# Kernel tuning notes

Hardware: AMD Instinct MI355X
Metric: run time of the kernel (lower is better)

The kernel has to match this reference:

```python
import jax, jax.numpy as jnp
import numpy as np

B, D = 65536, 784          # batch, input features
H = 256                     # delegator feature (hidden) dim
L = 64                      # num_leaves (experts)
C = 10                      # num_classes


def setup_inputs() -> dict:
    key = jax.random.key(0)
    ks = jax.random.split(key, 7)
    s_in = 1.0 / np.sqrt(D)
    s_h = 1.0 / np.sqrt(H)
    return {
        "x": jax.random.normal(ks[0], (B, D), dtype=jnp.float32),
        "Wf": jax.random.normal(ks[1], (D, H), dtype=jnp.float32) * s_in,   # Node feature proj
        "bf": jnp.zeros((H,), dtype=jnp.float32),
        "Wr": jax.random.normal(ks[2], (D, L), dtype=jnp.float32) * s_in,   # Node router proj
        "br": jnp.zeros((L,), dtype=jnp.float32),
        "Wl": jax.random.normal(ks[3], (L, H, C), dtype=jnp.float32) * s_h,  # per-leaf linear
        "bl": jnp.zeros((L, C), dtype=jnp.float32),
    }


def reference(x, Wf, bf, Wr, br, Wl, bl):
    # Delegator (Node): features + routing probabilities
    features = jax.nn.relu(x @ Wf + bf)                 # [B, H]
    probs = jax.nn.softmax(x @ Wr + br, axis=1)         # [B, L]
    choices = jnp.argmax(probs, axis=1)                 # [B] top-1 leaf per sample
    # Per-sample leaf dispatch: gather each sample's leaf weights, then a
    # batched vec-mat product (memory-bound gather, low FLOP/byte).
    Wc = Wl[choices]                                    # [B, H, C]
    bc = bl[choices]                                    # [B, C]
    predictions = jnp.einsum("bh,bhc->bc", features, Wc) + bc  # [B, C]
    return predictions
```

## Files before the change

### kernel.cpp

```cpp
#include <hip/hip_runtime.h>
#include <stdint.h>

#define B_ROWS 65536
#define D_IN   784
#define H_DIM  256
#define L_LEAF 64
#define C_CLS  10
#define NSTEP  13
#define BTILE  40960
#define GAP_THRESH 0.03f

using f32x4    = __attribute__((ext_vector_type(4))) float;
using bf16x8   = __attribute__((ext_vector_type(8))) short;
using ushort8v = __attribute__((ext_vector_type(8))) unsigned short;
using ushort4v = __attribute__((ext_vector_type(4))) unsigned short;

#define O_FLAGCNT  0
#define O_CHOICES  4096
#define O_FLAGROWS (O_CHOICES + B_ROWS * 4)
#define O_WT       (O_FLAGROWS + B_ROWS * 4)
#define O_FEAT     (O_WT + NSTEP * BTILE)
#define O_WLB      (O_FEAT + (size_t)B_ROWS * H_DIM * 2)
#define WS_BASE    O_WLB
#define WS_FULL    (O_WLB + (size_t)L_LEAF * H_DIM * C_CLS * 2)

__device__ __forceinline__ unsigned short f2bf(float f) {
    union { float f; unsigned int u; } c; c.f = f;
    unsigned int u = c.u;
    return (unsigned short)((u + 0x7fffu + ((u >> 16) & 1u)) >> 16);
}
__device__ __forceinline__ float bf2f(unsigned short u) {
    union { unsigned int u; float f; } c; c.u = ((unsigned int)u) << 16;
    return c.f;
}
__device__ __forceinline__ unsigned int cvtpk(float a, float b) {
    unsigned int r;
    asm("v_cvt_pk_bf16_f32 %0, %1, %2" : "=v"(r) : "v"(a), "v"(b));
    return r;
}

__device__ __forceinline__ void gload_lds16(const void* g, void* l) {
    __builtin_amdgcn_global_load_lds(
        (const __attribute__((address_space(1))) unsigned int*)g,
        (__attribute__((address_space(3))) unsigned int*)l, 16, 0, 0);
}

__global__ void k0_prep(const float* __restrict__ Wf, const float* __restrict__ Wr,
                        unsigned short* __restrict__ Wt, unsigned int* __restrict__ flagcnt) {
    if (blockIdx.x == 0 && threadIdx.x == 0) *flagcnt = 0u;
    int id = blockIdx.x * 256 + threadIdx.x;
    int ts = id / 2560;
    int r  = id % 2560;
    int n  = r % 320;
    int c4 = r / 320;
    int ks = ts * 64 + ((c4 ^ (n & 7)) << 3);
    unsigned short v[8];
    #pragma unroll
    for (int j = 0; j < 8; ++j) {
        int k = ks + j;
        float f = 0.f;
        if (k < D_IN)
            f = (n < H_DIM) ? Wf[(size_t)k * H_DIM + n]
                            : Wr[(size_t)k * L_LEAF + (n - H_DIM)];
        v[j] = f2bf(f);
    }
    *(ushort8v*)((char*)Wt + (size_t)ts * BTILE + (size_t)(n * 8 + c4) * 16) = *(ushort8v*)v;
}

__global__ void k0b_wl(const float* __restrict__ Wl, unsigned short* __restrict__ Wlb) {
    int i = (blockIdx.x * 256 + threadIdx.x) * 4;
    f32x4 v = *(const f32x4*)(Wl + i);
    ushort4v h; h.x = f2bf(v.x); h.y = f2bf(v.y); h.z = f2bf(v.z); h.w = f2bf(v.w);
    *(ushort4v*)(Wlb + i) = h;
}

__global__ __launch_bounds__(256, 2) void k1_gemm(
    const float* __restrict__ x, const unsigned short* __restrict__ Wt,
    const float* __restrict__ bfv, const float* __restrict__ brv,
    unsigned short* __restrict__ feat, int* __restrict__ choices,
    unsigned int* __restrict__ flagcnt, int* __restrict__ flagrows)
{
    __shared__ __align__(16) unsigned short Bl[2][320 * 64];

    const int t = threadIdx.x, w = t >> 6, l = t & 63, q = l >> 4, ic = l & 15;
    const int bm0 = blockIdx.x * 64;
    const float* xbase = x + (size_t)(bm0 + ic) * D_IN;

    f32x4 acc[4][5];
    #pragma unroll
    for (int a = 0; a < 4; ++a)
        #pragma unroll
        for (int b = 0; b < 5; ++b)
            acc[a][b] = (f32x4){0.f, 0.f, 0.f, 0.f};

    const int rb0 = ic * 64 + (((q    ) ^ (ic & 7)) << 3);
    const int rb1 = ic * 64 + (((q + 4) ^ (ic & 7)) << 3);
    const int ntb = w * 5;

    #pragma unroll
    for (int i = 0; i < 10; ++i) {
        int cid = i * 256 + t;
        gload_lds16((const char*)Wt + cid * 16, (char*)&Bl[0][0] + cid * 16);
    }
    f32x4 an[4][4];
    #pragma unroll
    for (int mt = 0; mt < 4; ++mt) {
        const float* xr = xbase + (size_t)(mt * 16) * D_IN;
        #pragma unroll
        for (int kk = 0; kk < 2; ++kk) {
            int kg = kk * 32 + q * 8;
            an[mt][2 * kk]     = *(const f32x4*)(xr + kg);
            an[mt][2 * kk + 1] = *(const f32x4*)(xr + kg + 4);
        }
    }
    __syncthreads();

    int cur = 0;
    for (int ts = 0; ts < NSTEP; ++ts) {
        if (ts + 1 < NSTEP) {
            const char* src = (const char*)Wt + (size_t)(ts + 1) * BTILE;
            char* dst = (char*)&Bl[cur ^ 1][0];
            #pragma unroll
            for (int i = 0; i < 10; ++i) {
                int cid = i * 256 + t;
                gload_lds16(src + cid * 16, dst + cid * 16);
            }
        }
        bf16x8 af[4][2];
        #pragma unroll
        for (int mt = 0; mt < 4; ++mt) {
            #pragma unroll
            for (int kk = 0; kk < 2; ++kk) {
                union { unsigned int u[4]; bf16x8 v; } pk;
                f32x4 lo = an[mt][2 * kk], hi = an[mt][2 * kk + 1];
                pk.u[0] = cvtpk(lo.x, lo.y);
                pk.u[1] = cvtpk(lo.z, lo.w);
                pk.u[2] = cvtpk(hi.x, hi.y);
                pk.u[3] = cvtpk(hi.z, hi.w);
                af[mt][kk] = pk.v;
            }
        }
        if (ts + 1 < NSTEP) {
            #pragma unroll
            for (int mt = 0; mt < 4; ++mt) {
                const float* xr = xbase + (size_t)(mt * 16) * D_IN;
                #pragma unroll
                for (int kk = 0; kk < 2; ++kk) {
                    int kg = (ts + 1) * 64 + kk * 32 + q * 8;
                    if (kg + 8 <= D_IN) {
                        an[mt][2 * kk]     = *(const f32x4*)(xr + kg);
                        an[mt][2 * kk + 1] = *(const f32x4*)(xr + kg + 4);
                    } else {
                        an[mt][2 * kk]     = (f32x4){0.f, 0.f, 0.f, 0.f};
                        an[mt][2 * kk + 1] = (f32x4){0.f, 0.f, 0.f, 0.f};
                    }
                }
            }
        }
        const unsigned short* Bc = &Bl[cur][0];
        #pragma unroll
        for (int j = 0; j < 5; ++j) {
            bf16x8 b = *(const bf16x8*)(Bc + (ntb + j) * 1024 + rb0);
            #pragma unroll
            for (int mt = 0; mt < 4; ++mt)
                acc[mt][j] = __builtin_amdgcn_mfma_f32_16x16x32_bf16(af[mt][0], b, acc[mt][j], 0, 0, 0);
        }
        #pragma unroll
        for (int j = 0; j < 5; ++j) {
            bf16x8 b = *(const bf16x8*)(Bc + (ntb + j) * 1024 + rb1);
            #pragma unroll
            for (int mt = 0; mt < 4; ++mt)
                acc[mt][j] = __builtin_amdgcn_mfma_f32_16x16x32_bf16(af[mt][1], b, acc[mt][j], 0, 0, 0);
        }
        __syncthreads();
        cur ^= 1;
    }

    #pragma unroll
    for (int j = 0; j < 5; ++j) {
        int col = (ntb + j) * 16 + ic;
        if (col < H_DIM) {
            float bias = bfv[col];
            #pragma unroll
            for (int mt = 0; mt < 4; ++mt) {
                #pragma unroll
                for (int i = 0; i < 4; ++i) {
                    int row = bm0 + mt * 16 + q * 4 + i;
                    float v = acc[mt][j][i] + bias;
                    v = v > 0.f ? v : 0.f;
                    feat[(size_t)row * H_DIM + col] = f2bf(v);
                }
            }
        }
    }
    if (w == 3) {
        #pragma unroll
        for (int mt = 0; mt < 4; ++mt) {
            #pragma unroll
            for (int i = 0; i < 4; ++i) {
                float m1 = -1e30f, m2 = -1e30f;
                int a1 = 0;
                #pragma unroll
                for (int j = 1; j < 5; ++j) {
                    int leaf = (j - 1) * 16 + ic;
                    float v = acc[mt][j][i] + brv[leaf];
                    if (v > m1) { m2 = m1; m1 = v; a1 = leaf; }
                    else if (v > m2) { m2 = v; }
                }
                #pragma unroll
                for (int s = 1; s < 16; s <<= 1) {
                    float om1 = __shfl_xor(m1, s, 64);
                    float om2 = __shfl_xor(m2, s, 64);
                    int   oa1 = __shfl_xor(a1, s, 64);
                    bool take = (om1 > m1) || (om1 == m1 && oa1 < a1);
                    float nm2 = take ? fmaxf(om2, m1) : fmaxf(m2, om1);
                    m1 = take ? om1 : m1;
                    a1 = take ? oa1 : a1;
                    m2 = nm2;
                }
                if (ic == 0) {
                    int row = bm0 + mt * 16 + q * 4 + i;
                    choices[row] = a1;
                    if (m1 - m2 < GAP_THRESH) {
                        unsigned int idx = atomicAdd(flagcnt, 1u);
                        flagrows[idx] = row;
                    }
                }
            }
        }
    }
}

__global__ __launch_bounds__(256) void k2_exact(
    const float* __restrict__ x, const float* __restrict__ Wr,
    const float* __restrict__ brv, const unsigned int* __restrict__ flagcnt,
    const int* __restrict__ flagrows, int* __restrict__ choices)
{
    __shared__ float wl[64 * 64];
    __shared__ float xl[4][64];
    const unsigned int cnt = *flagcnt;
    const int t = threadIdx.x, w = t >> 6, l = t & 63;
    for (unsigned int base = blockIdx.x * 4u; base < cnt; base += gridDim.x * 4u) {
        unsigned int ri = base + w;
        int row = (ri < cnt) ? flagrows[ri] : 0;
        const float* xr = x + (size_t)row * D_IN;
        float s0 = 0.f, s1 = 0.f, s2 = 0.f, s3 = 0.f;
        for (int kt = 0; kt < NSTEP; ++kt) {
            int k0 = kt * 64;
            #pragma unroll
            for (int i = 0; i < 4; ++i) {
                int flat = i * 256 + t;
                int kk = flat >> 4, lq = (flat & 15) * 4;
                int kg = k0 + kk;
                f32x4 v = (f32x4){0.f, 0.f, 0.f, 0.f};
                if (kg < D_IN) v = *(const f32x4*)(Wr + (size_t)kg * L_LEAF + lq);
                *(f32x4*)&wl[kk * 64 + lq] = v;
            }
            xl[w][l] = (k0 + l < D_IN) ? xr[k0 + l] : 0.f;
            __syncthreads();
            #pragma unroll
            for (int kk = 0; kk < 64; kk += 4) {
                s0 = fmaf(xl[w][kk    ], wl[(kk    ) * 64 + l], s0);
                s1 = fmaf(xl[w][kk + 1], wl[(kk + 1) * 64 + l], s1);
                s2 = fmaf(xl[w][kk + 2], wl[(kk + 2) * 64 + l], s2);
                s3 = fmaf(xl[w][kk + 3], wl[(kk + 3) * 64 + l], s3);
            }
            __syncthreads();
        }
        float v = (s0 + s1) + (s2 + s3) + brv[l];
        int a = l;
        #pragma unroll
        for (int st = 1; st < 64; st <<= 1) {
            float ov = __shfl_xor(v, st, 64);
            int   oa = __shfl_xor(a, st, 64);
            if (ov > v || (ov == v && oa < a)) { v = ov; a = oa; }
        }
        if (l == 0 && ri < cnt) choices[row] = a;
    }
}

__global__ __launch_bounds__(256) void k3_leaf(
    const unsigned short* __restrict__ feat, const int* __restrict__ choices,
    const float* __restrict__ Wl, const unsigned short* __restrict__ Wlb,
    const float* __restrict__ blv, float* __restrict__ out)
{
    const int t = threadIdx.x, wv = t >> 6, l = t & 63, g = l >> 4, i = l & 15;
    const int row = blockIdx.x * 16 + wv * 4 + g;
    const int leaf = choices[row];

    ushort8v f0 = *(const ushort8v*)(feat + (size_t)row * H_DIM + i * 16);
    ushort8v f1 = *(const ushort8v*)(feat + (size_t)row * H_DIM + i * 16 + 8);
    float fv[16];
    #pragma unroll
    for (int j = 0; j < 8; ++j) { fv[j] = bf2f(f0[j]); fv[8 + j] = bf2f(f1[j]); }

    float acc[C_CLS];
    #pragma unroll
    for (int c = 0; c < C_CLS; ++c) acc[c] = 0.f;

    if (Wlb) {
        const unsigned short* wp = Wlb + ((size_t)leaf * H_DIM + i * 16) * C_CLS;
        ushort8v wreg[20];
        #pragma unroll
        for (int j = 0; j < 20; ++j) wreg[j] = *(const ushort8v*)(wp + j * 8);
        #pragma unroll
        for (int h = 0; h < 16; ++h) {
            #pragma unroll
            for (int c = 0; c < C_CLS; ++c) {
                int e = h * C_CLS + c;
                acc[c] = fmaf(fv[h], bf2f(wreg[e >> 3][e & 7]), acc[c]);
            }
        }
    } else {
        const float* wp = Wl + ((size_t)leaf * H_DIM + i * 16) * C_CLS;
        #pragma unroll
        for (int h = 0; h < 16; ++h) {
            #pragma unroll
            for (int c = 0; c < C_CLS; ++c)
                acc[c] = fmaf(fv[h], wp[h * C_CLS + c], acc[c]);
        }
    }
    #pragma unroll
    for (int st = 1; st < 16; st <<= 1) {
        #pragma unroll
        for (int c = 0; c < C_CLS; ++c) acc[c] += __shfl_xor(acc[c], st, 64);
    }
    if (i == 0) {
        #pragma unroll
        for (int c = 0; c < C_CLS; ++c)
            out[(size_t)row * C_CLS + c] = acc[c] + blv[leaf * C_CLS + c];
    }
}

extern "C" void kernel_launch(void* const* d_in, const int* in_sizes, int n_in,
                              void* d_out, int out_size, void* d_ws, size_t ws_size,
                              hipStream_t stream) {
    if (ws_size < WS_BASE) return;
    const bool use_bf = ws_size >= WS_FULL;

    const float* x   = (const float*)d_in[0];
    const float* Wf  = (const float*)d_in[1];
    const float* bfv = (const float*)d_in[2];
    const float* Wr  = (const float*)d_in[3];
    const float* brv = (const float*)d_in[4];
    const float* Wl  = (const float*)d_in[5];
    const float* blv = (const float*)d_in[6];
    float* out = (float*)d_out;

    char* ws = (char*)d_ws;
    unsigned int*   flagcnt  = (unsigned int*)(ws + O_FLAGCNT);
    int*            choices  = (int*)(ws + O_CHOICES);
    int*            flagrows = (int*)(ws + O_FLAGROWS);
    unsigned short* Wt       = (unsigned short*)(ws + O_WT);
    unsigned short* feat     = (unsigned short*)(ws + O_FEAT);
    unsigned short* Wlb      = use_bf ? (unsigned short*)(ws + O_WLB) : (unsigned short*)0;

    hipLaunchKernelGGL(k0_prep, dim3(130), dim3(256), 0, stream, Wf, Wr, Wt, flagcnt);
    if (use_bf)
        hipLaunchKernelGGL(k0b_wl, dim3(160), dim3(256), 0, stream, Wl, Wlb);
    hipLaunchKernelGGL(k1_gemm, dim3(B_ROWS / 64), dim3(256), 0, stream,
                       x, Wt, bfv, brv, feat, choices, flagcnt, flagrows);
    hipLaunchKernelGGL(k2_exact, dim3(1024), dim3(256), 0, stream,
                       x, Wr, brv, flagcnt, flagrows, choices);
    hipLaunchKernelGGL(k3_leaf, dim3(B_ROWS / 16), dim3(256), 0, stream,
                       feat, choices, Wl, Wlb, blv, out);
}
```

Before: 206.3 us.

## Halve GEMM K-tile to 32 and raise occupancy to four blocks per CU

Cuts the K step of the fused feature/router GEMM from 64 to 32, which halves the double-buffered LDS tile to 40 KB and lets launch bounds target four blocks per CU instead of two. The x register prefetch of the next K slice is dropped; each step now loads its own x slice directly before converting to bf16. The weight pre-pack kernel and its swizzle layout are changed to match the new tile. The intent is to hide memory latency through more resident waves rather than explicit software prefetch. In exchange there are twice as many barriers, and x loads are exposed within each step.

Result: slower. 211.7 us (+2.7%).

```diff
diff --git a/kernel.cpp b/kernel.cpp
--- a/kernel.cpp
+++ b/kernel.cpp
@@ -6,8 +6,8 @@
 #define H_DIM  256
 #define L_LEAF 64
 #define C_CLS  10
-#define NSTEP  13
-#define BTILE  40960
+#define NSTEP2 25
+#define BTILE2 20480
 #define GAP_THRESH 0.03f
 
 using f32x4    = __attribute__((ext_vector_type(4))) float;
@@ -19,7 +19,8 @@
 #define O_CHOICES  4096
 #define O_FLAGROWS (O_CHOICES + B_ROWS * 4)
 #define O_WT       (O_FLAGROWS + B_ROWS * 4)
-#define O_FEAT     (O_WT + NSTEP * BTILE)
+#define WT_BYTES   (NSTEP2 * BTILE2)
+#define O_FEAT     (O_WT + WT_BYTES)
 #define O_WLB      (O_FEAT + (size_t)B_ROWS * H_DIM * 2)
 #define WS_BASE    O_WLB
 #define WS_FULL    (O_WLB + (size_t)L_LEAF * H_DIM * C_CLS * 2)
@@ -49,11 +50,12 @@
                         unsigned short* __restrict__ Wt, unsigned int* __restrict__ flagcnt) {
     if (blockIdx.x == 0 && threadIdx.x == 0) *flagcnt = 0u;
     int id = blockIdx.x * 256 + threadIdx.x;
-    int ts = id / 2560;
-    int r  = id % 2560;
+    int ts = id / 1280;
+    int r  = id % 1280;
     int n  = r % 320;
-    int c4 = r / 320;
-    int ks = ts * 64 + ((c4 ^ (n & 7)) << 3);
+    int c  = r / 320;
+    int dst = ts * BTILE2 + ((n * 64 + c * 16) ^ ((n & 7) << 4));
+    int ks  = ts * 32 + c * 8;
     unsigned short v[8];
     #pragma unroll
     for (int j = 0; j < 8; ++j) {
@@ -64,7 +66,7 @@
                             : Wr[(size_t)k * L_LEAF + (n - H_DIM)];
         v[j] = f2bf(f);
     }
-    *(ushort8v*)((char*)Wt + (size_t)ts * BTILE + (size_t)(n * 8 + c4) * 16) = *(ushort8v*)v;
+    *(ushort8v*)((char*)Wt + dst) = *(ushort8v*)v;
 }
 
 __global__ void k0b_wl(const float* __restrict__ Wl, unsigned short* __restrict__ Wlb) {
@@ -74,13 +76,13 @@
     *(ushort4v*)(Wlb + i) = h;
 }
 
-__global__ __launch_bounds__(256, 2) void k1_gemm(
+__global__ __launch_bounds__(256, 4) void k1_gemm(
     const float* __restrict__ x, const unsigned short* __restrict__ Wt,
     const float* __restrict__ bfv, const float* __restrict__ brv,
     unsigned short* __restrict__ feat, int* __restrict__ choices,
     unsigned int* __restrict__ flagcnt, int* __restrict__ flagrows)
 {
-    __shared__ __align__(16) unsigned short Bl[2][320 * 64];
+    __shared__ __align__(16) unsigned short Bl[2][320 * 32];
 
     const int t = threadIdx.x, w = t >> 6, l = t & 63, q = l >> 4, ic = l & 15;
     const int bm0 = blockIdx.x * 64;
@@ -93,84 +95,55 @@
         for (int b = 0; b < 5; ++b)
             acc[a][b] = (f32x4){0.f, 0.f, 0.f, 0.f};
 
-    const int rb0 = ic * 64 + (((q    ) ^ (ic & 7)) << 3);
-    const int rb1 = ic * 64 + (((q + 4) ^ (ic & 7)) << 3);
+    const int rbB = (ic * 64 + (q << 4)) ^ ((ic & 7) << 4);
     const int ntb = w * 5;
 
     #pragma unroll
-    for (int i = 0; i < 10; ++i) {
+    for (int i = 0; i < 5; ++i) {
         int cid = i * 256 + t;
         gload_lds16((const char*)Wt + cid * 16, (char*)&Bl[0][0] + cid * 16);
     }
-    f32x4 an[4][4];
-    #pragma unroll
-    for (int mt = 0; mt < 4; ++mt) {
-        const float* xr = xbase + (size_t)(mt * 16) * D_IN;
-        #pragma unroll
-        for (int kk = 0; kk < 2; ++kk) {
-            int kg = kk * 32 + q * 8;
-            an[mt][2 * kk]     = *(const f32x4*)(xr + kg);
-            an[mt][2 * kk + 1] = *(const f32x4*)(xr + kg + 4);
-        }
-    }
     __syncthreads();
 
     int cur = 0;
-    for (int ts = 0; ts < NSTEP; ++ts) {
-        if (ts + 1 < NSTEP) {
-            const char* src = (const char*)Wt + (size_t)(ts + 1) * BTILE;
+    for (int ts = 0; ts < NSTEP2; ++ts) {
+        if (ts + 1 < NSTEP2) {
+            const char* src = (const char*)Wt + (size_t)(ts + 1) * BTILE2;
             char* dst = (char*)&Bl[cur ^ 1][0];
             #pragma unroll
-            for (int i = 0; i < 10; ++i) {
+            for (int i = 0; i < 5; ++i) {
                 int cid = i * 256 + t;
                 gload_lds16(src + cid * 16, dst + cid * 16);
             }
         }
-        bf16x8 af[4][2];
+        const int kg = ts * 32 + q * 8;
+        const bool ok = (kg + 8 <= D_IN);
+        const int kgs = ok ? kg : 0;
+        f32x4 an[4][2];
         #pragma unroll
         for (int mt = 0; mt < 4; ++mt) {
-            #pragma unroll
-            for (int kk = 0; kk < 2; ++kk) {
-                union { unsigned int u[4]; bf16x8 v; } pk;
-                f32x4 lo = an[mt][2 * kk], hi = an[mt][2 * kk + 1];
-                pk.u[0] = cvtpk(lo.x, lo.y);
-                pk.u[1] = cvtpk(lo.z, lo.w);
-                pk.u[2] = cvtpk(hi.x, hi.y);
-                pk.u[3] = cvtpk(hi.z, hi.w);
-                af[mt][kk] = pk.v;
-            }
-        }
-        if (ts + 1 < NSTEP) {
-            #pragma unroll
-            for (int mt = 0; mt < 4; ++mt) {
-                const float* xr = xbase + (size_t)(mt * 16) * D_IN;
-                #pragma unroll
-                for (int kk = 0; kk < 2; ++kk) {
-                    int kg = (ts + 1) * 64 + kk * 32 + q * 8;
-                    if (kg + 8 <= D_IN) {
-                        an[mt][2 * kk]     = *(const f32x4*)(xr + kg);
-                        an[mt][2 * kk + 1] = *(const f32x4*)(xr + kg + 4);
-                    } else {
-                        an[mt][2 * kk]     = (f32x4){0.f, 0.f, 0.f, 0.f};
-                        an[mt][2 * kk + 1] = (f32x4){0.f, 0.f, 0.f, 0.f};
-                    }
-                }
-            }
-        }
-        const unsigned short* Bc = &Bl[cur][0];
+            const float* xr = xbase + (size_t)(mt * 16) * D_IN + kgs;
+            an[mt][0] = *(const f32x4*)(xr);
+            an[mt][1] = *(const f32x4*)(xr + 4);
+        }
+        bf16x8 af[4];
+        #pragma unroll
+        for (int mt = 0; mt < 4; ++mt) {
+            union { unsigned int u[4]; bf16x8 v; } pk;
+            f32x4 lo = an[mt][0], hi = an[mt][1];
+            pk.u[0] = ok ? cvtpk(lo.x, lo.y) : 0u;
+            pk.u[1] = ok ? cvtpk(lo.z, lo.w) : 0u;
+            pk.u[2] = ok ? cvtpk(hi.x, hi.y) : 0u;
+            pk.u[3] = ok ? cvtpk(hi.z, hi.w) : 0u;
+            af[mt] = pk.v;
+        }
+        const char* Bc = (const char*)&Bl[cur][0];
         #pragma unroll
         for (int j = 0; j < 5; ++j) {
-            bf16x8 b = *(const bf16x8*)(Bc + (ntb + j) * 1024 + rb0);
+            bf16x8 b = *(const bf16x8*)(Bc + (ntb + j) * 1024 + rbB);
             #pragma unroll
             for (int mt = 0; mt < 4; ++mt)
-                acc[mt][j] = __builtin_amdgcn_mfma_f32_16x16x32_bf16(af[mt][0], b, acc[mt][j], 0, 0, 0);
-        }
-        #pragma unroll
-        for (int j = 0; j < 5; ++j) {
-            bf16x8 b = *(const bf16x8*)(Bc + (ntb + j) * 1024 + rb1);
-            #pragma unroll
-            for (int mt = 0; mt < 4; ++mt)
-                acc[mt][j] = __builtin_amdgcn_mfma_f32_16x16x32_bf16(af[mt][1], b, acc[mt][j], 0, 0, 0);
+                acc[mt][j] = __builtin_amdgcn_mfma_f32_16x16x32_bf16(af[mt], b, acc[mt][j], 0, 0, 0);
         }
         __syncthreads();
         cur ^= 1;
@@ -245,15 +218,15 @@
         int row = (ri < cnt) ? flagrows[ri] : 0;
         const float* xr = x + (size_t)row * D_IN;
         float s0 = 0.f, s1 = 0.f, s2 = 0.f, s3 = 0.f;
-        for (int kt = 0; kt < NSTEP; ++kt) {
+        for (int kt = 0; kt < 13; ++kt) {
             int k0 = kt * 64;
             #pragma unroll
             for (int i = 0; i < 4; ++i) {
                 int flat = i * 256 + t;
                 int kk = flat >> 4, lq = (flat & 15) * 4;
-                int kg = k0 + kk;
+                int kgk = k0 + kk;
                 f32x4 v = (f32x4){0.f, 0.f, 0.f, 0.f};
-                if (kg < D_IN) v = *(const f32x4*)(Wr + (size_t)kg * L_LEAF + lq);
+                if (kgk < D_IN) v = *(const f32x4*)(Wr + (size_t)kgk * L_LEAF + lq);
                 *(f32x4*)&wl[kk * 64 + lq] = v;
             }
             xl[w][l] = (k0 + l < D_IN) ? xr[k0 + l] : 0.f;
@@ -355,7 +328,7 @@
     unsigned short* feat     = (unsigned short*)(ws + O_FEAT);
     unsigned short* Wlb      = use_bf ? (unsigned short*)(ws + O_WLB) : (unsigned short*)0;
 
-    hipLaunchKernelGGL(k0_prep, dim3(130), dim3(256), 0, stream, Wf, Wr, Wt, flagcnt);
+    hipLaunchKernelGGL(k0_prep, dim3(125), dim3(256), 0, stream, Wf, Wr, Wt, flagcnt);
     if (use_bf)
         hipLaunchKernelGGL(k0b_wl, dim3(160), dim3(256), 0, stream, Wl, Wlb);
     hipLaunchKernelGGL(k1_gemm, dim3(B_ROWS / 64), dim3(256), 0, stream,
```
